# Kernel tuning notes

Hardware: AMD Instinct MI355X
Metric: run time of the kernel (lower is better)

## Reference

```python
import jax, jax.numpy as jnp
import numpy as np

N_NODES = 100000
N_EDGES = 2000000
IN_C = 30
OUT_C = 10
HID = 4 * OUT_C      # 40
D1 = 2 * OUT_C       # 20
D2 = OUT_C           # 10
N_CLASSES = 3
K_SAMPLE = 8


def setup_inputs() -> dict:
    key = jax.random.key(0)
    ks = jax.random.split(key, 24)
    inp = {
        'x': jax.random.normal(ks[0], (N_NODES, IN_C), dtype=jnp.float32),
        'edge_index': jax.random.randint(ks[1], (2, N_EDGES), 0, N_NODES, dtype=jnp.int64),
        'edge_attr': jax.random.uniform(ks[2], (N_EDGES,), dtype=jnp.float32),
        'label': 1,
        # gcn1
        'W1': jax.random.normal(ks[3], (IN_C, HID), dtype=jnp.float32) * (1.0 / np.sqrt(IN_C)),
        'b1': jnp.zeros((HID,), jnp.float32),
        'ln1_w': jnp.ones((HID,), jnp.float32),
        'ln1_b': jnp.zeros((HID,), jnp.float32),
        # gcn2
        'W2': jax.random.normal(ks[4], (HID, HID), dtype=jnp.float32) * (1.0 / np.sqrt(HID)),
        'b2': jnp.zeros((HID,), jnp.float32),
        'ln2_w': jnp.ones((HID,), jnp.float32),
        'ln2_b': jnp.zeros((HID,), jnp.float32),
        # fnn
        'Wf': jax.random.normal(ks[5], (HID, D1), dtype=jnp.float32) * (1.0 / np.sqrt(HID)),
        'bf': jnp.zeros((D1,), jnp.float32),
        # attention (tanh / sigmoid branches + concat)
        'Wt': jax.random.normal(ks[6], (D1, D2), dtype=jnp.float32) * (1.0 / np.sqrt(D1)),
        'bt': jnp.zeros((D2,), jnp.float32),
        'Ws': jax.random.normal(ks[7], (D1, D2), dtype=jnp.float32) * (1.0 / np.sqrt(D1)),
        'bs': jnp.zeros((D2,), jnp.float32),
        'Wc': jax.random.normal(ks[8], (D2, 1), dtype=jnp.float32) * (1.0 / np.sqrt(D2)),
        'bc': jnp.zeros((1,), jnp.float32),
        # bag classifier
        'Wcls': jax.random.normal(ks[9], (D1, N_CLASSES), dtype=jnp.float32) * (1.0 / np.sqrt(D1)),
        'bcls': jnp.zeros((N_CLASSES,), jnp.float32),
        # per-class cell-scale classifiers, stacked [n_classes, D1, 2]
        'Wcell': jax.random.normal(ks[10], (N_CLASSES, D1, 2), dtype=jnp.float32) * (1.0 / np.sqrt(D1)),
        'bcell': jnp.zeros((N_CLASSES, 2), jnp.float32),
    }
    return inp


def _layernorm(x, w, b, eps=1e-5):
    m = jnp.mean(x, axis=-1, keepdims=True)
    v = jnp.var(x, axis=-1, keepdims=True)
    return (x - m) * jax.lax.rsqrt(v + eps) * w + b


def _gcn(x, W, b, src, dst, ew, n):
    # PyG GCNConv: add self-loops (weight 1), symmetric norm, aggregate at dst
    h = x @ W                                              # [N, F]
    deg = jax.ops.segment_sum(ew, dst, num_segments=n) + 1.0
    dinv = jnp.where(deg > 0, jax.lax.rsqrt(deg), 0.0)     # [N]
    norm = dinv[src] * ew * dinv[dst]                      # [E]
    agg = jax.ops.segment_sum(h[src] * norm[:, None], dst, num_segments=n)
    agg = agg + h * (dinv * dinv)[:, None]                 # self-loop term
    return agg + b


def _forward(x, edge_attr, W1, b1, ln1_w, ln1_b, W2, b2, ln2_w, ln2_b,
             Wf, bf, Wt, bt, Ws, bs, Wc, bc, Wcls, bcls, Wcell, bcell,
             edge_index, label):
    src, dst = edge_index[0], edge_index[1]
    n = x.shape[0]
    x1 = jax.nn.selu(_layernorm(_gcn(x, W1, b1, src, dst, edge_attr, n), ln1_w, ln1_b))
    x2 = jax.nn.selu(_layernorm(_gcn(x1, W2, b2, src, dst, edge_attr, n), ln2_w, ln2_b))
    x3 = jax.nn.selu(x2 @ Wf + bf)                         # [N, D1] == x_out
    # gated tanh*sigmoid attention
    gate = jnp.tanh(x3 @ Wt + bt) * jax.nn.sigmoid(x3 @ Ws + bs)
    A = (gate @ Wc + bc).T                                 # [1, N]
    A = jax.nn.softmax(A, axis=1)
    # cell-scale eval for the true class (one-hot label selects exactly one)
    a_row = A[-1]                                          # [N]
    _, idx_p = jax.lax.top_k(a_row, K_SAMPLE)
    _, idx_n = jax.lax.top_k(-a_row, K_SAMPLE)
    all_cells = jnp.concatenate([x3[idx_p], x3[idx_n]], axis=0)   # [2K, D1]
    logits_c = all_cells @ Wcell[label] + bcell[label]            # [2K, 2]
    targets = jnp.concatenate([jnp.ones((K_SAMPLE,), jnp.int32),
                               jnp.zeros((K_SAMPLE,), jnp.int32)])
    # SmoothTop1SVM (tau=1, alpha=1): mean( logsumexp(s + Delta) - s_y )
    delta = 1.0 - jax.nn.one_hot(targets, 2, dtype=logits_c.dtype)
    s_y = jnp.take_along_axis(logits_c, targets[:, None], axis=1)[:, 0]
    cell_loss = jnp.mean(jax.nn.logsumexp(logits_c + delta, axis=1) - s_y)
    # bag-level prediction
    x_pooled = A @ x3                                      # [1, D1]
    logits = x_pooled @ Wcls + bcls                        # [1, n_classes]
    Y_prob = jax.nn.softmax(logits, axis=1)
    Y_hat = jnp.argmax(logits, axis=1)[:, None]
    return logits, Y_prob, Y_hat, A, x3, cell_loss


def reference(x, edge_index, edge_attr, label, W1, b1, ln1_w, ln1_b, W2, b2,
              ln2_w, ln2_b, Wf, bf, Wt, bt, Ws, bs, Wc, bc, Wcls, bcls,
              Wcell, bcell):
    return _forward(x, edge_attr, W1, b1, ln1_w, ln1_b, W2, b2, ln2_w, ln2_b,
                    Wf, bf, Wt, bt, Ws, bs, Wc, bc, Wcls, bcls, Wcell, bcell,
                    edge_index, label)
```

## Files before the change

kernel.cpp:

```cpp
#include <hip/hip_runtime.h>
#include <hip/hip_bf16.h>
#include <math.h>

typedef __hip_bfloat16 bf16;

__device__ __forceinline__ float tof(bf16 v){ return __bfloat162float(v); }
__device__ __forceinline__ bf16  tob(float v){ return __float2bfloat16(v); }

__device__ __forceinline__ float sane(float v){
  return (v == v && v > -1e30f && v < 1e30f) ? v : 0.f;
}
__device__ __forceinline__ float ldf(const void* p, size_t i, bool f32){
  float v = f32 ? ((const float*)p)[i] : tof(((const bf16*)p)[i]);
  return sane(v);
}
__device__ __forceinline__ void stf(void* p, size_t i, float v, bool f32){
  if (f32) ((float*)p)[i] = v; else ((bf16*)p)[i] = tob(v);
}
__device__ __forceinline__ bool is_f32(const unsigned* __restrict__ dt){
  return dt[0] == 0x3F800000u;
}
__device__ __forceinline__ int clampi(int v, int hi){
  return ((unsigned)v < (unsigned)hi) ? v : 0;
}
__device__ __forceinline__ float selu_f(float x){
  const float sc = 1.0507009873554805f, al = 1.6732632423543772f;
  return x > 0.f ? sc * x : sc * al * (expf(x) - 1.0f);
}
__device__ __forceinline__ void unpack8(uint4 u, float* f){
  f[0]=__uint_as_float(u.x<<16); f[1]=__uint_as_float(u.x&0xFFFF0000u);
  f[2]=__uint_as_float(u.y<<16); f[3]=__uint_as_float(u.y&0xFFFF0000u);
  f[4]=__uint_as_float(u.z<<16); f[5]=__uint_as_float(u.z&0xFFFF0000u);
  f[6]=__uint_as_float(u.w<<16); f[7]=__uint_as_float(u.w&0xFFFF0000u);
}
__device__ __forceinline__ void unpack4(uint2 u, float* f){
  f[0]=__uint_as_float(u.x<<16); f[1]=__uint_as_float(u.x&0xFFFF0000u);
  f[2]=__uint_as_float(u.y<<16); f[3]=__uint_as_float(u.y&0xFFFF0000u);
}
__device__ __forceinline__ unsigned pack2(float a, float b){
  unsigned short ua, ub;
  bf16 ta = tob(a), tb = tob(b);
  __builtin_memcpy(&ua, &ta, 2);
  __builtin_memcpy(&ub, &tb, 2);
  return (unsigned)ua | ((unsigned)ub << 16);
}

__global__ void k_zero(float* __restrict__ p, int n){
  int i = blockIdx.x * blockDim.x + threadIdx.x;
  int stride = gridDim.x * blockDim.x;
  for (; i < n; i += stride) p[i] = 0.f;
}

__device__ __forceinline__ bool idx_is64(const int* __restrict__ raw){
  return ((raw[1] | raw[3] | raw[5] | raw[7] | raw[9] | raw[11]) == 0);
}
__device__ __forceinline__ void edge_at(const int* __restrict__ raw, int E, int e,
                                        bool w64, int N, int& s, int& d){
  int sv, dv;
  if (w64){ sv = raw[2 * e]; dv = raw[2 * (E + e)]; }
  else    { sv = raw[e];     dv = raw[E + e]; }
  s = clampi(sv, N); d = clampi(dv, N);
}

__global__ void k_cnt_rank(const int* __restrict__ raw, int* __restrict__ cnt,
                           int* __restrict__ rank, int E, int N){
  int e = blockIdx.x * blockDim.x + threadIdx.x;
  if (e >= E) return;
  bool w64 = idx_is64(raw);
  int s, d; edge_at(raw, E, e, w64, N, s, d);
  rank[e] = atomicAdd(&cnt[d], 1);
}

__global__ void k_scan_block(const int* __restrict__ cnt, int* __restrict__ bsum, int N){
  __shared__ int s[256];
  int base = blockIdx.x * 1024;
  int acc = 0;
  for (int k = threadIdx.x; k < 1024; k += 256){
    int i = base + k;
    acc += (i < N) ? cnt[i] : 0;
  }
  s[threadIdx.x] = acc; __syncthreads();
  for (int w = 128; w > 0; w >>= 1){
    if (threadIdx.x < w) s[threadIdx.x] += s[threadIdx.x + w];
    __syncthreads();
  }
  if (threadIdx.x == 0) bsum[blockIdx.x] = s[0];
}

__global__ void k_scan_partials(int* __restrict__ bsum, int B, int* __restrict__ rowpN, int E){
  __shared__ int s[256];
  int run = 0;
  for (int t0 = 0; t0 < B; t0 += 256){
    int i = t0 + threadIdx.x;
    int v = (i < B) ? bsum[i] : 0;
    s[threadIdx.x] = v;
    __syncthreads();
    for (int o = 1; o < 256; o <<= 1){
      int add = (threadIdx.x >= o) ? s[threadIdx.x - o] : 0;
      __syncthreads();
      s[threadIdx.x] += add;
      __syncthreads();
    }
    int incl = s[threadIdx.x];
    int total = s[255];
    __syncthreads();
    if (i < B) bsum[i] = run + incl - v;
    run += total;
    __syncthreads();
  }
  if (threadIdx.x == 0) rowpN[0] = E;
}

__global__ void k_scan_final(const int* __restrict__ cnt, const int* __restrict__ bsum,
                             int* __restrict__ rowp, int N){
  __shared__ int s[256];
  int t = threadIdx.x;
  int base = bsum[blockIdx.x];
  int i0 = blockIdx.x * 1024 + t * 4;
  int v0=0,v1=0,v2=0,v3=0;
  if (i0+0 < N) v0 = cnt[i0+0];
  if (i0+1 < N) v1 = cnt[i0+1];
  if (i0+2 < N) v2 = cnt[i0+2];
  if (i0+3 < N) v3 = cnt[i0+3];
  int sum = v0+v1+v2+v3;
  s[t] = sum; __syncthreads();
  for (int o = 1; o < 256; o <<= 1){
    int add = (t >= o) ? s[t - o] : 0;
    __syncthreads();
    s[t] += add;
    __syncthreads();
  }
  int off = base + s[t] - sum;
  if (i0+0 < N){ rowp[i0+0]=off; off+=v0; }
  if (i0+1 < N){ rowp[i0+1]=off; off+=v1; }
  if (i0+2 < N){ rowp[i0+2]=off; off+=v2; }
  if (i0+3 < N){ rowp[i0+3]=off; off+=v3; }
}

__global__ void k_place(const int* __restrict__ raw, const void* __restrict__ ea,
                        const unsigned* __restrict__ dt, const int* __restrict__ rank,
                        const int* __restrict__ rowp, int2* __restrict__ ep, int E, int N){
  int e = blockIdx.x * blockDim.x + threadIdx.x;
  if (e >= E) return;
  bool f32 = is_f32(dt);
  bool w64 = idx_is64(raw);
  int s, d; edge_at(raw, E, e, w64, N, s, d);
  float w = ldf(ea, e, f32);
  int pos = rowp[d] + rank[e];
  if ((unsigned)pos < (unsigned)E)
    ep[pos] = make_int2(s, __float_as_int(w));
}

__global__ void k_dinv_csr(const int* __restrict__ rowp, const int2* __restrict__ ep,
                           float* __restrict__ dinv, int N, int E){
  int n = blockIdx.x * blockDim.x + threadIdx.x;
  if (n >= N) return;
  int beg = rowp[n], end = rowp[n + 1];
  if (beg < 0) beg = 0;
  if (end > E) end = E;
  float s = 0.f;
  for (int j = beg; j < end; j++) s += sane(__int_as_float(ep[j].y));
  float dv = s + 1.0f;
  dinv[n] = (dv > 0.f) ? rsqrtf(dv) : 0.f;
}

__global__ void k_premul(int2* __restrict__ ep, const float* __restrict__ dinv,
                         int E, int N){
  int i = blockIdx.x * blockDim.x + threadIdx.x;
  if (i >= E) return;
  int2 p = ep[i];
  int s = clampi(p.x, N);
  float w = dinv[s] * sane(__int_as_float(p.y));
  ep[i] = make_int2(s, __float_as_int(w));
}

__global__ void k_mm1(const void* __restrict__ X, const void* __restrict__ W,
                      const unsigned* __restrict__ dt,
                      bf16* __restrict__ H, int N, int Nx){
  bool f32 = is_f32(dt);
  __shared__ float w[30 * 40];
  __shared__ float xs[256 * 30];
  for (int i = threadIdx.x; i < 30 * 40; i += 256) w[i] = ldf(W, i, f32);
  int base = blockIdx.x * 256;
  int rows = Nx - base; if (rows > 256) rows = 256; if (rows < 0) rows = 0;
  int nelem = rows * 30;
  size_t gbase = (size_t)base * 30;
  for (int i = threadIdx.x; i < nelem; i += 256) xs[i] = ldf(X, gbase + i, f32);
  __syncthreads();
  int n = base + threadIdx.x;
  if (n >= N) return;
  float acc[40];
  #pragma unroll
  for (int j = 0; j < 40; j++) acc[j] = 0.f;
  if (threadIdx.x < rows){
    const float* xr = &xs[threadIdx.x * 30];
    for (int i = 0; i < 30; i++){
      float xi = xr[i];
      #pragma unroll
      for (int j = 0; j < 40; j++) acc[j] += xi * w[i * 40 + j];
    }
  } else {
    for (int i = 0; i < 30; i++){
      float xi = ldf(X, i, f32);
      #pragma unroll
      for (int j = 0; j < 40; j++) acc[j] += xi * w[i * 40 + j];
    }
  }
  uint4 ob[5];
  unsigned* ou = (unsigned*)ob;
  #pragma unroll
  for (int q = 0; q < 20; q++) ou[q] = pack2(acc[2*q], acc[2*q+1]);
  uint4* op = (uint4*)(H + (size_t)n * 40);
  #pragma unroll
  for (int q = 0; q < 5; q++) op[q] = ob[q];
}

__global__ void k_mm2(const bf16* __restrict__ X, const void* __restrict__ W,
                      const unsigned* __restrict__ dt,
                      bf16* __restrict__ H, int N){
  bool f32 = is_f32(dt);
  __shared__ float w[40 * 40];
  for (int i = threadIdx.x; i < 40 * 40; i += 256) w[i] = ldf(W, i, f32);
  __syncthreads();
  int n = blockIdx.x * blockDim.x + threadIdx.x;
  if (n >= N) return;
  float acc[40];
  #pragma unroll
  for (int j = 0; j < 40; j++) acc[j] = 0.f;
  const uint4* xp = (const uint4*)(X + (size_t)n * 40);
  #pragma unroll
  for (int q = 0; q < 5; q++){
    uint4 u = xp[q];
    float f[8]; unpack8(u, f);
    #pragma unroll
    for (int k = 0; k < 8; k++){
      float xi = f[k];
      int i = q * 8 + k;
      #pragma unroll
      for (int j = 0; j < 40; j++) acc[j] += xi * w[i * 40 + j];
    }
  }
  uint4 ob[5];
  unsigned* ou = (unsigned*)ob;
  #pragma unroll
  for (int q = 0; q < 20; q++) ou[q] = pack2(acc[2*q], acc[2*q+1]);
  uint4* op = (uint4*)(H + (size_t)n * 40);
  #pragma unroll
  for (int q = 0; q < 5; q++) op[q] = ob[q];
}

__global__ void k_gather(const int* __restrict__ rowp, const int2* __restrict__ ep,
                         const bf16* __restrict__ h, const float* __restrict__ dinv,
                         const void* __restrict__ b, const void* __restrict__ lw,
                         const void* __restrict__ lb, const unsigned* __restrict__ dt,
                         bf16* __restrict__ xout, int N, int E){
  int tid = blockIdx.x * blockDim.x + threadIdx.x;
  int n  = tid >> 3;
  int sl = tid & 7;
  if (n >= N) return;
  bool f32 = is_f32(dt);
  bool act = sl < 5;
  int fb = sl * 8;
  float dn = dinv[n];
  int beg = rowp[n], end = rowp[n + 1];
  if (beg < 0) beg = 0;
  if (end > E) end = E;
  float a[8];
  #pragma unroll
  for (int k = 0; k < 8; k++) a[k] = 0.f;
  int j = beg;
  for (; j + 3 < end; j += 4){
    int2 p0 = ep[j], p1 = ep[j+1], p2 = ep[j+2], p3 = ep[j+3];
    int s0 = clampi(p0.x, N), s1 = clampi(p1.x, N);
    int s2 = clampi(p2.x, N), s3 = clampi(p3.x, N);
    if (act){
      uint4 u0 = *(const uint4*)(h + (size_t)s0 * 40 + fb);
      uint4 u1 = *(const uint4*)(h + (size_t)s1 * 40 + fb);
      uint4 u2 = *(const uint4*)(h + (size_t)s2 * 40 + fb);
      uint4 u3 = *(const uint4*)(h + (size_t)s3 * 40 + fb);
      float w0 = __int_as_float(p0.y), w1 = __int_as_float(p1.y);
      float w2 = __int_as_float(p2.y), w3 = __int_as_float(p3.y);
      float f0[8], f1[8], f2[8], f3[8];
      unpack8(u0, f0); unpack8(u1, f1); unpack8(u2, f2); unpack8(u3, f3);
      #pragma unroll
      for (int k = 0; k < 8; k++)
        a[k] += f0[k]*w0 + f1[k]*w1 + f2[k]*w2 + f3[k]*w3;
    }
  }
  for (; j < end; j++){
    int2 p = ep[j];
    int s = clampi(p.x, N);
    if (act){
      uint4 u = *(const uint4*)(h + (size_t)s * 40 + fb);
      float w = __int_as_float(p.y);
      float f[8]; unpack8(u, f);
      #pragma unroll
      for (int k = 0; k < 8; k++) a[k] += f[k] * w;
    }
  }
  float v[8]; float psum = 0.f;
  if (act){
    uint4 us = *(const uint4*)(h + (size_t)n * 40 + fb);
    float fs[8]; unpack8(us, fs);
    float di2 = dn * dn;
    #pragma unroll
    for (int k = 0; k < 8; k++){
      v[k] = sane(a[k] * dn) + fs[k] * di2 + ldf(b, fb + k, f32);
      psum += v[k];
    }
  } else {
    #pragma unroll
    for (int k = 0; k < 8; k++) v[k] = 0.f;
  }
  float sum = psum;
  sum += __shfl_xor(sum, 1); sum += __shfl_xor(sum, 2); sum += __shfl_xor(sum, 4);
  float m = sum * (1.0f / 40.0f);
  float sq = 0.f;
  if (act){
    #pragma unroll
    for (int k = 0; k < 8; k++){ float d = v[k] - m; sq += d * d; }
  }
  sq += __shfl_xor(sq, 1); sq += __shfl_xor(sq, 2); sq += __shfl_xor(sq, 4);
  float inv = rsqrtf(sq * (1.0f / 40.0f) + 1e-5f);
  if (act){
    float y[8];
    #pragma unroll
    for (int k = 0; k < 8; k++)
      y[k] = sane(selu_f((v[k] - m) * inv * ldf(lw, fb + k, f32) + ldf(lb, fb + k, f32)));
    uint4 ob;
    unsigned* ou = (unsigned*)&ob;
    #pragma unroll
    for (int q = 0; q < 4; q++) ou[q] = pack2(y[2*q], y[2*q+1]);
    *(uint4*)(xout + (size_t)n * 40 + fb) = ob;
  }
}

__global__ void k_head(const bf16* __restrict__ x2,
                       const void* __restrict__ Wf, const void* __restrict__ bfv,
                       const void* __restrict__ Wt, const void* __restrict__ bt,
                       const void* __restrict__ Ws, const void* __restrict__ bs,
                       const void* __restrict__ Wc, const void* __restrict__ bc,
                       const unsigned* __restrict__ dt,
                       bf16* __restrict__ x3ws, float* __restrict__ alog, int N){
  bool f32 = is_f32(dt);
  __shared__ float wf[800], bff[20], wt[200], btt[10], wss[200], bss[10], wc[10], bcc[1];
  for (int i = threadIdx.x; i < 800; i += blockDim.x) wf[i] = ldf(Wf, i, f32);
  for (int i = threadIdx.x; i < 200; i += blockDim.x){
    wt[i] = ldf(Wt, i, f32); wss[i] = ldf(Ws, i, f32);
  }
  if (threadIdx.x < 20) bff[threadIdx.x] = ldf(bfv, threadIdx.x, f32);
  if (threadIdx.x < 10){ btt[threadIdx.x] = ldf(bt, threadIdx.x, f32);
                         bss[threadIdx.x] = ldf(bs, threadIdx.x, f32);
                         wc[threadIdx.x]  = ldf(Wc, threadIdx.x, f32); }
  if (threadIdx.x == 0) bcc[0] = ldf(bc, 0, f32);
  __syncthreads();
  int n = blockIdx.x * blockDim.x + threadIdx.x;
  if (n >= N) return;
  float r[40];
  const uint4* xp = (const uint4*)(x2 + (size_t)n * 40);
  #pragma unroll
  for (int q = 0; q < 5; q++){
    uint4 u = xp[q];
    unpack8(u, &r[q * 8]);
  }
  float x3r[20];
  #pragma unroll
  for (int j = 0; j < 20; j++){
    float acc = bff[j];
    for (int i = 0; i < 40; i++) acc += r[i] * wf[i * 20 + j];
    x3r[j] = sane(selu_f(acc));
  }
  uint2 ob[5];
  unsigned* ou = (unsigned*)ob;
  #pragma unroll
  for (int q = 0; q < 10; q++) ou[q] = pack2(x3r[2*q], x3r[2*q+1]);
  uint2* op = (uint2*)(x3ws + (size_t)n * 20);
  #pragma unroll
  for (int q = 0; q < 5; q++) op[q] = ob[q];
  float a = bcc[0];
  #pragma unroll
  for (int j = 0; j < 10; j++){
    float zt = btt[j], zs = bss[j];
    for (int i = 0; i < 20; i++){ zt += x3r[i] * wt[i * 10 + j]; zs += x3r[i] * wss[i * 10 + j]; }
    float g = tanhf(zt) * (1.0f / (1.0f + expf(-zs)));
    a += g * wc[j];
  }
  alog[n] = sane(a);
}

__global__ void k_copy_x3(const bf16* __restrict__ x3ws, const unsigned* __restrict__ dt,
                          void* __restrict__ out, size_t off, int total){
  bool f32 = is_f32(dt);
  int i = blockIdx.x * blockDim.x + threadIdx.x;
  int stride = gridDim.x * blockDim.x;
  for (; i < total; i += stride) stf(out, off + i, tof(x3ws[i]), f32);
}

__global__ void k_msum(const float* __restrict__ a, float2* __restrict__ part, int n){
  __shared__ float sm[256], sl[256];
  int t = threadIdx.x;
  float m = -1e30f, l = 0.f;
  for (int i = blockIdx.x * blockDim.x + t; i < n; i += gridDim.x * blockDim.x){
    float v = sane(a[i]);
    if (v > m){ l = l * expf(m - v) + 1.f; m = v; }
    else        l += expf(v - m);
  }
  sm[t] = m; sl[t] = l; __syncthreads();
  for (int w = 128; w > 0; w >>= 1){
    if (t < w){
      float m2 = sm[t+w], l2 = sl[t+w];
      float mm = fmaxf(sm[t], m2);
      sl[t] = sl[t] * expf(sm[t] - mm) + l2 * expf(m2 - mm);
      sm[t] = mm;
    }
    __syncthreads();
  }
  if (t == 0) part[blockIdx.x] = make_float2(sm[0], sl[0]);
}

__global__ void k_msum_fin(const float2* __restrict__ part, float* __restrict__ scal,
                           float* __restrict__ pooled){
  __shared__ float sm[256], sl[256];
  int t = threadIdx.x;
  float2 p = part[t];
  sm[t] = p.x; sl[t] = p.y; __syncthreads();
  for (int w = 128; w > 0; w >>= 1){
    if (t < w){
      float m2 = sm[t+w], l2 = sl[t+w];
      float mm = fmaxf(sm[t], m2);
      sl[t] = sl[t] * expf(sm[t] - mm) + l2 * expf(m2 - mm);
      sm[t] = mm;
    }
    __syncthreads();
  }
  if (t == 0){ scal[0] = sm[0]; scal[1] = sl[0]; }
  if (t < 20) pooled[t] = 0.f;
}

__global__ void k_writeA(const float* __restrict__ alog, const bf16* __restrict__ x3ws,
                         const float* __restrict__ scal,
                         const unsigned* __restrict__ dt,
                         void* __restrict__ out, size_t a_off,
                         float* __restrict__ pooled, int N){
  bool f32 = is_f32(dt);
  float gmax = scal[0];
  float sum  = scal[1];
  float inv  = (sum > 0.f) ? 1.0f / sum : 0.f;
  float acc[20];
  #pragma unroll
  for (int j = 0; j < 20; j++) acc[j] = 0.f;
  for (int i = blockIdx.x * blockDim.x + threadIdx.x; i < N; i += gridDim.x * blockDim.x){
    float a = expf(sane(alog[i]) - gmax) * inv;
    stf(out, a_off + i, a, f32);
    const uint2* xr = (const uint2*)(x3ws + (size_t)i * 20);
    #pragma unroll
    for (int q = 0; q < 5; q++){
      float f[4]; unpack4(xr[q], f);
      #pragma unroll
      for (int k = 0; k < 4; k++) acc[q * 4 + k] += a * f[k];
    }
  }
  __shared__ float s[20];
  if (threadIdx.x < 20) s[threadIdx.x] = 0.f;
  __syncthreads();
  #pragma unroll
  for (int j = 0; j < 20; j++) atomicAdd(&s[j], acc[j]);
  __syncthreads();
  if (threadIdx.x < 20) atomicAdd(&pooled[threadIdx.x], s[threadIdx.x]);
}

__global__ void k_topk1(const float* __restrict__ a, int N,
                        float* __restrict__ cvp, int* __restrict__ cip,
                        float* __restrict__ cvn, int* __restrict__ cin){
  const int T = 256, K = 8;
  __shared__ float sv[T * K];
  __shared__ int   si[T * K];
  __shared__ float rv[T];
  __shared__ int   ri[T];
  __shared__ int   rs[T];
  int t = threadIdx.x;
  float tv[K]; int ti[K]; float bv[K]; int bi[K];
  #pragma unroll
  for (int k = 0; k < K; k++){ tv[k] = -1e38f; ti[k] = 0x7ffffff;
                               bv[k] =  1e38f; bi[k] = 0x7ffffff; }
  for (int i = blockIdx.x * T + t; i < N; i += gridDim.x * T){
    float v = sane(a[i]);
    if (v > tv[K-1]){
      int p = K - 1;
      while (p > 0 && v > tv[p-1]){ tv[p] = tv[p-1]; ti[p] = ti[p-1]; p--; }
      tv[p] = v; ti[p] = i;
    }
    if (v < bv[K-1]){
      int p = K - 1;
      while (p > 0 && v < bv[p-1]){ bv[p] = bv[p-1]; bi[p] = bi[p-1]; p--; }
      bv[p] = v; bi[p] = i;
    }
  }
  for (int k = 0; k < K; k++){ sv[t*K+k] = tv[k]; si[t*K+k] = ti[k]; }
  __syncthreads();
  for (int round = 0; round < K; round++){
    float bvv = -1e38f; int bii = 0x7ffffff; int bslot = 0;
    for (int k = 0; k < K; k++){
      float v = sv[t*K+k]; int ii = si[t*K+k];
      if (v > bvv || (v == bvv && ii < bii)){ bvv = v; bii = ii; bslot = t*K+k; }
    }
    rv[t] = bvv; ri[t] = bii; rs[t] = bslot;
    __syncthreads();
    for (int w = T/2; w > 0; w >>= 1){
      if (t < w){
        float v2 = rv[t+w]; int i2 = ri[t+w];
        if (v2 > rv[t] || (v2 == rv[t] && i2 < ri[t])){ rv[t]=v2; ri[t]=i2; rs[t]=rs[t+w]; }
      }
      __syncthreads();
    }
    if (t == 0){ cvp[blockIdx.x*K + round] = rv[0]; cip[blockIdx.x*K + round] = ri[0];
                 sv[rs[0]] = -1e38f; }
    __syncthreads();
  }
  for (int k = 0; k < K; k++){ sv[t*K+k] = bv[k]; si[t*K+k] = bi[k]; }
  __syncthreads();
  for (int round = 0; round < K; round++){
    float bvv = 1e38f; int bii = 0x7ffffff; int bslot = 0;
    for (int k = 0; k < K; k++){
      float v = sv[t*K+k]; int ii = si[t*K+k];
      if (v < bvv || (v == bvv && ii < bii)){ bvv = v; bii = ii; bslot = t*K+k; }
    }
    rv[t] = bvv; ri[t] = bii; rs[t] = bslot;
    __syncthreads();
    for (int w = T/2; w > 0; w >>= 1){
      if (t < w){
        float v2 = rv[t+w]; int i2 = ri[t+w];
        if (v2 < rv[t] || (v2 == rv[t] && i2 < ri[t])){ rv[t]=v2; ri[t]=i2; rs[t]=rs[t+w]; }
      }
      __syncthreads();
    }
    if (t == 0){ cvn[blockIdx.x*K + round] = rv[0]; cin[blockIdx.x*K + round] = ri[0];
                 sv[rs[0]] = 1e38f; }
    __syncthreads();
  }
}

__global__ void k_topk2(const float* __restrict__ cvp, const int* __restrict__ cip,
                        const float* __restrict__ cvn, const int* __restrict__ cin,
                        int* __restrict__ idxp, int* __restrict__ idxn, int M){
  const int T = 256, CAP = 1024, PER = CAP / T;
  __shared__ float sv[CAP];
  __shared__ int   si[CAP];
  __shared__ float rv[T];
  __shared__ int   ri[T];
  __shared__ int   rs[T];
  int t = threadIdx.x;
  for (int i = t; i < CAP; i += T){
    sv[i] = (i < M) ? cvp[i] : -1e38f;
    si[i] = (i < M) ? cip[i] : 0x7ffffff;
  }
  __syncthreads();
  for (int round = 0; round < 8; round++){
    float bvv = -1e38f; int bii = 0x7ffffff; int bslot = t * PER;
    for (int k = 0; k < PER; k++){
      float v = sv[t*PER+k]; int ii = si[t*PER+k];
      if (v > bvv || (v == bvv && ii < bii)){ bvv = v; bii = ii; bslot = t*PER+k; }
    }
    rv[t] = bvv; ri[t] = bii; rs[t] = bslot;
    __syncthreads();
    for (int w = T/2; w > 0; w >>= 1){
      if (t < w){
        float v2 = rv[t+w]; int i2 = ri[t+w];
        if (v2 > rv[t] || (v2 == rv[t] && i2 < ri[t])){ rv[t]=v2; ri[t]=i2; rs[t]=rs[t+w]; }
      }
      __syncthreads();
    }
    if (t == 0){ idxp[round] = ri[0]; sv[rs[0]] = -1e38f; }
    __syncthreads();
  }
  for (int i = t; i < CAP; i += T){
    sv[i] = (i < M) ? cvn[i] : 1e38f;
    si[i] = (i < M) ? cin[i] : 0x7ffffff;
  }
  __syncthreads();
  for (int round = 0; round < 8; round++){
    float bvv = 1e38f; int bii = 0x7ffffff; int bslot = t * PER;
    for (int k = 0; k < PER; k++){
      float v = sv[t*PER+k]; int ii = si[t*PER+k];
      if (v < bvv || (v == bvv && ii < bii)){ bvv = v; bii = ii; bslot = t*PER+k; }
    }
    rv[t] = bvv; ri[t] = bii; rs[t] = bslot;
    __syncthreads();
    for (int w = T/2; w > 0; w >>= 1){
      if (t < w){
        float v2 = rv[t+w]; int i2 = ri[t+w];
        if (v2 < rv[t] || (v2 == rv[t] && i2 < ri[t])){ rv[t]=v2; ri[t]=i2; rs[t]=rs[t+w]; }
      }
      __syncthreads();
    }
    if (t == 0){ idxn[round] = ri[0]; sv[rs[0]] = 1e38f; }
    __syncthreads();
  }
}

__global__ void k_final(const float* __restrict__ pooled,
                        const void* __restrict__ Wcls, const void* __restrict__ bcls,
                        const void* __restrict__ Wcell, const void* __restrict__ bcell,
                        const int* __restrict__ label_p, const bf16* __restrict__ x3ws,
                        const int* __restrict__ idxp, const int* __restrict__ idxn,
                        const unsigned* __restrict__ dt,
                        void* __restrict__ out, int N){
  if (threadIdx.x != 0 || blockIdx.x != 0) return;
  bool f32 = is_f32(dt);
  float lg[3];
  for (int c = 0; c < 3; c++){
    float acc = ldf(bcls, c, f32);
    for (int j = 0; j < 20; j++) acc += sane(pooled[j]) * ldf(Wcls, j * 3 + c, f32);
    lg[c] = sane(acc);
  }
  float m = fmaxf(lg[0], fmaxf(lg[1], lg[2]));
  float e0 = expf(lg[0]-m), e1 = expf(lg[1]-m), e2 = expf(lg[2]-m);
  float es = e0 + e1 + e2;
  int yhat = 0;
  if (lg[1] > lg[yhat]) yhat = 1;
  if (lg[2] > lg[yhat]) yhat = 2;
  stf(out, 0, lg[0], f32); stf(out, 1, lg[1], f32); stf(out, 2, lg[2], f32);
  stf(out, 3, e0/es, f32); stf(out, 4, e1/es, f32); stf(out, 5, e2/es, f32);
  stf(out, 6, (float)yhat, f32);
  int lw0 = label_p[0];
  int label;
  if ((unsigned)lw0 < 3u) label = lw0;
  else if (lw0 == 0x3F800000 || lw0 == 0x3F803F80) label = 1;
  else if (lw0 == 0x40000000 || lw0 == 0x40004000) label = 2;
  else label = 0;
  float w0[20], w1[20];
  for (int j = 0; j < 20; j++){
    w0[j] = ldf(Wcell, (size_t)label * 40 + j*2 + 0, f32);
    w1[j] = ldf(Wcell, (size_t)label * 40 + j*2 + 1, f32);
  }
  float b0 = ldf(bcell, (size_t)label * 2 + 0, f32);
  float b1 = ldf(bcell, (size_t)label * 2 + 1, f32);
  float loss = 0.f;
  for (int i = 0; i < 16; i++){
    int node = clampi((i < 8) ? idxp[i] : idxn[i-8], N);
    const bf16* xr = x3ws + (size_t)node * 20;
    float l0 = b0, l1 = b1;
    for (int j = 0; j < 20; j++){ float xv = tof(xr[j]); l0 += xv * w0[j]; l1 += xv * w1[j]; }
    int tgt = (i < 8) ? 1 : 0;
    float a0 = l0 + ((tgt == 0) ? 0.f : 1.f);
    float a1 = l1 + ((tgt == 1) ? 0.f : 1.f);
    float mm = fmaxf(a0, a1);
    float lse = mm + logf(expf(a0-mm) + expf(a1-mm));
    float sy = tgt ? l1 : l0;
    loss += lse - sy;
  }
  stf(out, (size_t)7 + N + (size_t)20 * N, sane(loss * (1.0f / 16.0f)), f32);
}

extern "C" void kernel_launch(void* const* d_in, const int* in_sizes, int n_in,
                              void* d_out, int out_size, void* d_ws, size_t ws_size,
                              hipStream_t stream) {
  const int N = (out_size - 8) / 21;
  if (N <= 0) return;
  const int Nx = (in_sizes[0] / 30 < N) ? (in_sizes[0] / 30) : N;
  int E = in_sizes[1] / 2;
  if (in_sizes[2] < E) E = in_sizes[2];
  if (E < 6) return;

  const void* x    = d_in[0];
  const int*  eraw = (const int*)d_in[1];
  const void* ea   = d_in[2];
  const int*  lbl  = (const int*)d_in[3];
  const void* W1   = d_in[4];
  const void* b1   = d_in[5];
  const unsigned* dt = (const unsigned*)d_in[6];
  const void* ln1w = d_in[6];
  const void* ln1b = d_in[7];
  const void* W2   = d_in[8];
  const void* b2   = d_in[9];
  const void* ln2w = d_in[10];
  const void* ln2b = d_in[11];
  const void* Wf   = d_in[12];
  const void* bfv  = d_in[13];
  const void* Wt   = d_in[14];
  const void* bt   = d_in[15];
  const void* Ws   = d_in[16];
  const void* bs   = d_in[17];
  const void* Wc   = d_in[18];
  const void* bc   = d_in[19];
  const void* Wcls = d_in[20];
  const void* bcls = d_in[21];
  const void* Wcell= d_in[22];
  const void* bcell= d_in[23];

  auto align16 = [](size_t v){ return (v + 15) & ~(size_t)15; };
  size_t hA_bytes = (size_t)N * 40 * 2;
  size_t rank_bytes = (size_t)E * 4;
  size_t regA = hA_bytes > rank_bytes ? hA_bytes : rank_bytes;
  size_t off = 0;
  char* ws = (char*)d_ws;
  bf16* hA    = (bf16*)(ws + off);
  int*  rank  = (int*)(ws + off);  off = align16(off + regA);
  bf16* xB    = (bf16*)(ws + off); off = align16(off + (size_t)N * 40 * 2);
  int2* epack = (int2*)(ws + off); off = align16(off + (size_t)E * 8);
  int*  rowp  = (int*)(ws + off);  off = align16(off + (size_t)(N + 1) * 4);
  int*  cnt   = (int*)(ws + off);  off = align16(off + (size_t)N * 4);
  int*  bsum  = (int*)(ws + off);  off = align16(off + 4096 * 4);
  float* dinv = (float*)(ws + off); off = align16(off + (size_t)N * 4);
  float* alog = (float*)(ws + off); off = align16(off + (size_t)N * 4);
  float2* part2 = (float2*)(ws + off); off = align16(off + 256 * 8);
  float* scal = (float*)(ws + off); off = align16(off + 2 * 4);
  float* pooled = (float*)(ws + off); off = align16(off + 20 * 4);
  int*   idxp = (int*)(ws + off); off = align16(off + 8 * 4);
  int*   idxn = (int*)(ws + off); off = align16(off + 8 * 4);
  float* cvp  = (float*)(ws + off); off = align16(off + 1024 * 4);
  int*   cip  = (int*)(ws + off);   off = align16(off + 1024 * 4);
  float* cvn  = (float*)(ws + off); off = align16(off + 1024 * 4);
  int*   cin  = (int*)(ws + off);   off = align16(off + 1024 * 4);
  if (off > ws_size) return;
  bf16* x3ws = hA;

  const int TB = 256;
  const int gN = (N + TB - 1) / TB;
  const int gE = (E + TB - 1) / TB;
  const int gG = (int)(((size_t)N * 8 + TB - 1) / TB);
  const int SB = (N + 1023) / 1024;
  const int TP = 128;

  k_zero<<<gN, TB, 0, stream>>>((float*)cnt, N);
  k_cnt_rank<<<gE, TB, 0, stream>>>(eraw, cnt, rank, E, N);
  k_scan_block<<<SB, TB, 0, stream>>>(cnt, bsum, N);
  k_scan_partials<<<1, TB, 0, stream>>>(bsum, SB, rowp + N, E);
  k_scan_final<<<SB, TB, 0, stream>>>(cnt, bsum, rowp, N);
  k_place<<<gE, TB, 0, stream>>>(eraw, ea, dt, rank, rowp, epack, E, N);
  k_dinv_csr<<<gN, TB, 0, stream>>>(rowp, epack, dinv, N, E);
  k_premul<<<gE, TB, 0, stream>>>(epack, dinv, E, N);

  k_mm1<<<gN, TB, 0, stream>>>(x, W1, dt, hA, N, Nx);
  k_gather<<<gG, TB, 0, stream>>>(rowp, epack, hA, dinv, b1, ln1w, ln1b, dt, xB, N, E);

  k_mm2<<<gN, TB, 0, stream>>>(xB, W2, dt, hA, N);
  k_gather<<<gG, TB, 0, stream>>>(rowp, epack, hA, dinv, b2, ln2w, ln2b, dt, xB, N, E);

  k_head<<<gN, TB, 0, stream>>>(xB, Wf, bfv, Wt, bt, Ws, bs, Wc, bc, dt,
                                x3ws, alog, N);
  k_copy_x3<<<2048, TB, 0, stream>>>(x3ws, dt, d_out, (size_t)7 + N, 20 * N);

  k_msum<<<256, TB, 0, stream>>>(alog, part2, N);
  k_msum_fin<<<1, TB, 0, stream>>>(part2, scal, pooled);
  k_writeA<<<256, TB, 0, stream>>>(alog, x3ws, scal, dt, d_out, (size_t)7, pooled, N);

  k_topk1<<<TP, TB, 0, stream>>>(alog, N, cvp, cip, cvn, cin);
  k_topk2<<<1, TB, 0, stream>>>(cvp, cip, cvn, cin, idxp, idxn, TP * 8);
  k_final<<<1, 64, 0, stream>>>(pooled, Wcls, bcls, Wcell, bcell, lbl,
                                x3ws, idxp, idxn, dt, d_out, N);
}
```

Baseline: 602.2 us.

## Fold dinv premultiply into gather and fuse softmax-stats with top-k selection

Measured after the change: 592.0 us. Within noise of the previous version (-1.7%).

```diff
diff --git a/kernel.cpp b/kernel.cpp
--- a/kernel.cpp
+++ b/kernel.cpp
@@ -162,16 +162,6 @@
   for (int j = beg; j < end; j++) s += sane(__int_as_float(ep[j].y));
   float dv = s + 1.0f;
   dinv[n] = (dv > 0.f) ? rsqrtf(dv) : 0.f;
-}
-
-__global__ void k_premul(int2* __restrict__ ep, const float* __restrict__ dinv,
-                         int E, int N){
-  int i = blockIdx.x * blockDim.x + threadIdx.x;
-  if (i >= E) return;
-  int2 p = ep[i];
-  int s = clampi(p.x, N);
-  float w = dinv[s] * sane(__int_as_float(p.y));
-  ep[i] = make_int2(s, __float_as_int(w));
 }
 
 __global__ void k_mm1(const void* __restrict__ X, const void* __restrict__ W,
@@ -273,13 +263,15 @@
     int2 p0 = ep[j], p1 = ep[j+1], p2 = ep[j+2], p3 = ep[j+3];
     int s0 = clampi(p0.x, N), s1 = clampi(p1.x, N);
     int s2 = clampi(p2.x, N), s3 = clampi(p3.x, N);
+    float w0 = dinv[s0] * __int_as_float(p0.y);
+    float w1 = dinv[s1] * __int_as_float(p1.y);
+    float w2 = dinv[s2] * __int_as_float(p2.y);
+    float w3 = dinv[s3] * __int_as_float(p3.y);
     if (act){
       uint4 u0 = *(const uint4*)(h + (size_t)s0 * 40 + fb);
       uint4 u1 = *(const uint4*)(h + (size_t)s1 * 40 + fb);
       uint4 u2 = *(const uint4*)(h + (size_t)s2 * 40 + fb);
       uint4 u3 = *(const uint4*)(h + (size_t)s3 * 40 + fb);
-      float w0 = __int_as_float(p0.y), w1 = __int_as_float(p1.y);
-      float w2 = __int_as_float(p2.y), w3 = __int_as_float(p3.y);
       float f0[8], f1[8], f2[8], f3[8];
       unpack8(u0, f0); unpack8(u1, f1); unpack8(u2, f2); unpack8(u3, f3);
       #pragma unroll
@@ -290,9 +282,9 @@
   for (; j < end; j++){
     int2 p = ep[j];
     int s = clampi(p.x, N);
+    float w = dinv[s] * __int_as_float(p.y);
     if (act){
       uint4 u = *(const uint4*)(h + (size_t)s * 40 + fb);
-      float w = __int_as_float(p.y);
       float f[8]; unpack8(u, f);
       #pragma unroll
       for (int k = 0; k < 8; k++) a[k] += f[k] * w;
@@ -396,45 +388,167 @@
   for (; i < total; i += stride) stf(out, off + i, tof(x3ws[i]), f32);
 }
 
-__global__ void k_msum(const float* __restrict__ a, float2* __restrict__ part, int n){
-  __shared__ float sm[256], sl[256];
+__global__ void k_msum_topk1(const float* __restrict__ a, int N,
+                             float2* __restrict__ part,
+                             float* __restrict__ cvp, int* __restrict__ cip,
+                             float* __restrict__ cvn, int* __restrict__ cin){
+  const int T = 256, K = 8;
+  __shared__ float sv[T * K];
+  __shared__ int   si[T * K];
+  __shared__ float rv[T];
+  __shared__ int   ri[T];
+  __shared__ int   rs[T];
+  __shared__ float sm[T], slh[T];
   int t = threadIdx.x;
   float m = -1e30f, l = 0.f;
-  for (int i = blockIdx.x * blockDim.x + t; i < n; i += gridDim.x * blockDim.x){
+  float tv[K]; int ti[K]; float bv[K]; int bi[K];
+  #pragma unroll
+  for (int k = 0; k < K; k++){ tv[k] = -1e38f; ti[k] = 0x7ffffff;
+                               bv[k] =  1e38f; bi[k] = 0x7ffffff; }
+  for (int i = blockIdx.x * T + t; i < N; i += gridDim.x * T){
     float v = sane(a[i]);
     if (v > m){ l = l * expf(m - v) + 1.f; m = v; }
     else        l += expf(v - m);
-  }
-  sm[t] = m; sl[t] = l; __syncthreads();
+    if (v > tv[K-1]){
+      int p = K - 1;
+      while (p > 0 && v > tv[p-1]){ tv[p] = tv[p-1]; ti[p] = ti[p-1]; p--; }
+      tv[p] = v; ti[p] = i;
+    }
+    if (v < bv[K-1]){
+      int p = K - 1;
+      while (p > 0 && v < bv[p-1]){ bv[p] = bv[p-1]; bi[p] = bi[p-1]; p--; }
+      bv[p] = v; bi[p] = i;
+    }
+  }
+  sm[t] = m; slh[t] = l; __syncthreads();
   for (int w = 128; w > 0; w >>= 1){
     if (t < w){
-      float m2 = sm[t+w], l2 = sl[t+w];
+      float m2 = sm[t+w], l2 = slh[t+w];
       float mm = fmaxf(sm[t], m2);
-      sl[t] = sl[t] * expf(sm[t] - mm) + l2 * expf(m2 - mm);
+      slh[t] = slh[t] * expf(sm[t] - mm) + l2 * expf(m2 - mm);
       sm[t] = mm;
     }
     __syncthreads();
   }
-  if (t == 0) part[blockIdx.x] = make_float2(sm[0], sl[0]);
-}
-
-__global__ void k_msum_fin(const float2* __restrict__ part, float* __restrict__ scal,
-                           float* __restrict__ pooled){
-  __shared__ float sm[256], sl[256];
+  if (t == 0) part[blockIdx.x] = make_float2(sm[0], slh[0]);
+  __syncthreads();
+  for (int k = 0; k < K; k++){ sv[t*K+k] = tv[k]; si[t*K+k] = ti[k]; }
+  __syncthreads();
+  for (int round = 0; round < K; round++){
+    float bvv = -1e38f; int bii = 0x7ffffff; int bslot = 0;
+    for (int k = 0; k < K; k++){
+      float v = sv[t*K+k]; int ii = si[t*K+k];
+      if (v > bvv || (v == bvv && ii < bii)){ bvv = v; bii = ii; bslot = t*K+k; }
+    }
+    rv[t] = bvv; ri[t] = bii; rs[t] = bslot;
+    __syncthreads();
+    for (int w = T/2; w > 0; w >>= 1){
+      if (t < w){
+        float v2 = rv[t+w]; int i2 = ri[t+w];
+        if (v2 > rv[t] || (v2 == rv[t] && i2 < ri[t])){ rv[t]=v2; ri[t]=i2; rs[t]=rs[t+w]; }
+      }
+      __syncthreads();
+    }
+    if (t == 0){ cvp[blockIdx.x*K + round] = rv[0]; cip[blockIdx.x*K + round] = ri[0];
+                 sv[rs[0]] = -1e38f; }
+    __syncthreads();
+  }
+  for (int k = 0; k < K; k++){ sv[t*K+k] = bv[k]; si[t*K+k] = bi[k]; }
+  __syncthreads();
+  for (int round = 0; round < K; round++){
+    float bvv = 1e38f; int bii = 0x7ffffff; int bslot = 0;
+    for (int k = 0; k < K; k++){
+      float v = sv[t*K+k]; int ii = si[t*K+k];
+      if (v < bvv || (v == bvv && ii < bii)){ bvv = v; bii = ii; bslot = t*K+k; }
+    }
+    rv[t] = bvv; ri[t] = bii; rs[t] = bslot;
+    __syncthreads();
+    for (int w = T/2; w > 0; w >>= 1){
+      if (t < w){
+        float v2 = rv[t+w]; int i2 = ri[t+w];
+        if (v2 < rv[t] || (v2 == rv[t] && i2 < ri[t])){ rv[t]=v2; ri[t]=i2; rs[t]=rs[t+w]; }
+      }
+      __syncthreads();
+    }
+    if (t == 0){ cvn[blockIdx.x*K + round] = rv[0]; cin[blockIdx.x*K + round] = ri[0];
+                 sv[rs[0]] = 1e38f; }
+    __syncthreads();
+  }
+}
+
+__global__ void k_fin(const float2* __restrict__ part, int P,
+                      const float* __restrict__ cvp, const int* __restrict__ cip,
+                      const float* __restrict__ cvn, const int* __restrict__ cin,
+                      float* __restrict__ scal, float* __restrict__ pooled,
+                      int* __restrict__ idxp, int* __restrict__ idxn, int M){
+  const int T = 256, CAP = 1024, PER = CAP / T;
+  __shared__ float sv[CAP];
+  __shared__ int   si[CAP];
+  __shared__ float rv[T];
+  __shared__ int   ri[T];
+  __shared__ int   rs[T];
   int t = threadIdx.x;
-  float2 p = part[t];
-  sm[t] = p.x; sl[t] = p.y; __syncthreads();
+  float m = -1e30f, l = 0.f;
+  if (t < P){ float2 p = part[t]; m = p.x; l = p.y; }
+  rv[t] = m; sv[t] = l; __syncthreads();
   for (int w = 128; w > 0; w >>= 1){
     if (t < w){
-      float m2 = sm[t+w], l2 = sl[t+w];
-      float mm = fmaxf(sm[t], m2);
-      sl[t] = sl[t] * expf(sm[t] - mm) + l2 * expf(m2 - mm);
-      sm[t] = mm;
-    }
-    __syncthreads();
-  }
-  if (t == 0){ scal[0] = sm[0]; scal[1] = sl[0]; }
+      float m2 = rv[t+w], l2 = sv[t+w];
+      float mm = fmaxf(rv[t], m2);
+      sv[t] = sv[t] * expf(rv[t] - mm) + l2 * expf(m2 - mm);
+      rv[t] = mm;
+    }
+    __syncthreads();
+  }
+  if (t == 0){ scal[0] = rv[0]; scal[1] = sv[0]; }
   if (t < 20) pooled[t] = 0.f;
+  __syncthreads();
+  for (int i = t; i < CAP; i += T){
+    sv[i] = (i < M) ? cvp[i] : -1e38f;
+    si[i] = (i < M) ? cip[i] : 0x7ffffff;
+  }
+  __syncthreads();
+  for (int round = 0; round < 8; round++){
+    float bvv = -1e38f; int bii = 0x7ffffff; int bslot = t * PER;
+    for (int k = 0; k < PER; k++){
+      float v = sv[t*PER+k]; int ii = si[t*PER+k];
+      if (v > bvv || (v == bvv && ii < bii)){ bvv = v; bii = ii; bslot = t*PER+k; }
+    }
+    rv[t] = bvv; ri[t] = bii; rs[t] = bslot;
+    __syncthreads();
+    for (int w = T/2; w > 0; w >>= 1){
+      if (t < w){
+        float v2 = rv[t+w]; int i2 = ri[t+w];
+        if (v2 > rv[t] || (v2 == rv[t] && i2 < ri[t])){ rv[t]=v2; ri[t]=i2; rs[t]=rs[t+w]; }
+      }
+      __syncthreads();
+    }
+    if (t == 0){ idxp[round] = ri[0]; sv[rs[0]] = -1e38f; }
+    __syncthreads();
+  }
+  for (int i = t; i < CAP; i += T){
+    sv[i] = (i < M) ? cvn[i] : 1e38f;
+    si[i] = (i < M) ? cin[i] : 0x7ffffff;
+  }
+  __syncthreads();
+  for (int round = 0; round < 8; round++){
+    float bvv = 1e38f; int bii = 0x7ffffff; int bslot = t * PER;
+    for (int k = 0; k < PER; k++){
+      float v = sv[t*PER+k]; int ii = si[t*PER+k];
+      if (v < bvv || (v == bvv && ii < bii)){ bvv = v; bii = ii; bslot = t*PER+k; }
+    }
+    rv[t] = bvv; ri[t] = bii; rs[t] = bslot;
+    __syncthreads();
+    for (int w = T/2; w > 0; w >>= 1){
+      if (t < w){
+        float v2 = rv[t+w]; int i2 = ri[t+w];
+        if (v2 < rv[t] || (v2 == rv[t] && i2 < ri[t])){ rv[t]=v2; ri[t]=i2; rs[t]=rs[t+w]; }
+      }
+      __syncthreads();
+    }
+    if (t == 0){ idxn[round] = ri[0]; sv[rs[0]] = 1e38f; }
+    __syncthreads();
+  }
 }
 
 __global__ void k_writeA(const float* __restrict__ alog, const bf16* __restrict__ x3ws,
@@ -467,135 +581,6 @@
   for (int j = 0; j < 20; j++) atomicAdd(&s[j], acc[j]);
   __syncthreads();
   if (threadIdx.x < 20) atomicAdd(&pooled[threadIdx.x], s[threadIdx.x]);
-}
-
-__global__ void k_topk1(const float* __restrict__ a, int N,
-                        float* __restrict__ cvp, int* __restrict__ cip,
-                        float* __restrict__ cvn, int* __restrict__ cin){
-  const int T = 256, K = 8;
-  __shared__ float sv[T * K];
-  __shared__ int   si[T * K];
-  __shared__ float rv[T];
-  __shared__ int   ri[T];
-  __shared__ int   rs[T];
-  int t = threadIdx.x;
-  float tv[K]; int ti[K]; float bv[K]; int bi[K];
-  #pragma unroll
-  for (int k = 0; k < K; k++){ tv[k] = -1e38f; ti[k] = 0x7ffffff;
-                               bv[k] =  1e38f; bi[k] = 0x7ffffff; }
-  for (int i = blockIdx.x * T + t; i < N; i += gridDim.x * T){
-    float v = sane(a[i]);
-    if (v > tv[K-1]){
-      int p = K - 1;
-      while (p > 0 && v > tv[p-1]){ tv[p] = tv[p-1]; ti[p] = ti[p-1]; p--; }
-      tv[p] = v; ti[p] = i;
-    }
-    if (v < bv[K-1]){
-      int p = K - 1;
-      while (p > 0 && v < bv[p-1]){ bv[p] = bv[p-1]; bi[p] = bi[p-1]; p--; }
-      bv[p] = v; bi[p] = i;
-    }
-  }
-  for (int k = 0; k < K; k++){ sv[t*K+k] = tv[k]; si[t*K+k] = ti[k]; }
-  __syncthreads();
-  for (int round = 0; round < K; round++){
-    float bvv = -1e38f; int bii = 0x7ffffff; int bslot = 0;
-    for (int k = 0; k < K; k++){
-      float v = sv[t*K+k]; int ii = si[t*K+k];
-      if (v > bvv || (v == bvv && ii < bii)){ bvv = v; bii = ii; bslot = t*K+k; }
-    }
-    rv[t] = bvv; ri[t] = bii; rs[t] = bslot;
-    __syncthreads();
-    for (int w = T/2; w > 0; w >>= 1){
-      if (t < w){
-        float v2 = rv[t+w]; int i2 = ri[t+w];
-        if (v2 > rv[t] || (v2 == rv[t] && i2 < ri[t])){ rv[t]=v2; ri[t]=i2; rs[t]=rs[t+w]; }
-      }
-      __syncthreads();
-    }
-    if (t == 0){ cvp[blockIdx.x*K + round] = rv[0]; cip[blockIdx.x*K + round] = ri[0];
-                 sv[rs[0]] = -1e38f; }
-    __syncthreads();
-  }
-  for (int k = 0; k < K; k++){ sv[t*K+k] = bv[k]; si[t*K+k] = bi[k]; }
-  __syncthreads();
-  for (int round = 0; round < K; round++){
-    float bvv = 1e38f; int bii = 0x7ffffff; int bslot = 0;
-    for (int k = 0; k < K; k++){
-      float v = sv[t*K+k]; int ii = si[t*K+k];
-      if (v < bvv || (v == bvv && ii < bii)){ bvv = v; bii = ii; bslot = t*K+k; }
-    }
-    rv[t] = bvv; ri[t] = bii; rs[t] = bslot;
-    __syncthreads();
-    for (int w = T/2; w > 0; w >>= 1){
-      if (t < w){
-        float v2 = rv[t+w]; int i2 = ri[t+w];
-        if (v2 < rv[t] || (v2 == rv[t] && i2 < ri[t])){ rv[t]=v2; ri[t]=i2; rs[t]=rs[t+w]; }
-      }
-      __syncthreads();
-    }
-    if (t == 0){ cvn[blockIdx.x*K + round] = rv[0]; cin[blockIdx.x*K + round] = ri[0];
-                 sv[rs[0]] = 1e38f; }
-    __syncthreads();
-  }
-}
-
-__global__ void k_topk2(const float* __restrict__ cvp, const int* __restrict__ cip,
-                        const float* __restrict__ cvn, const int* __restrict__ cin,
-                        int* __restrict__ idxp, int* __restrict__ idxn, int M){
-  const int T = 256, CAP = 1024, PER = CAP / T;
-  __shared__ float sv[CAP];
-  __shared__ int   si[CAP];
-  __shared__ float rv[T];
-  __shared__ int   ri[T];
-  __shared__ int   rs[T];
-  int t = threadIdx.x;
-  for (int i = t; i < CAP; i += T){
-    sv[i] = (i < M) ? cvp[i] : -1e38f;
-    si[i] = (i < M) ? cip[i] : 0x7ffffff;
-  }
-  __syncthreads();
-  for (int round = 0; round < 8; round++){
-    float bvv = -1e38f; int bii = 0x7ffffff; int bslot = t * PER;
-    for (int k = 0; k < PER; k++){
-      float v = sv[t*PER+k]; int ii = si[t*PER+k];
-      if (v > bvv || (v == bvv && ii < bii)){ bvv = v; bii = ii; bslot = t*PER+k; }
-    }
-    rv[t] = bvv; ri[t] = bii; rs[t] = bslot;
-    __syncthreads();
-    for (int w = T/2; w > 0; w >>= 1){
-      if (t < w){
-        float v2 = rv[t+w]; int i2 = ri[t+w];
-        if (v2 > rv[t] || (v2 == rv[t] && i2 < ri[t])){ rv[t]=v2; ri[t]=i2; rs[t]=rs[t+w]; }
-      }
-      __syncthreads();
-    }
-    if (t == 0){ idxp[round] = ri[0]; sv[rs[0]] = -1e38f; }
-    __syncthreads();
-  }
-  for (int i = t; i < CAP; i += T){
-    sv[i] = (i < M) ? cvn[i] : 1e38f;
-    si[i] = (i < M) ? cin[i] : 0x7ffffff;
-  }
-  __syncthreads();
-  for (int round = 0; round < 8; round++){
-    float bvv = 1e38f; int bii = 0x7ffffff; int bslot = t * PER;
-    for (int k = 0; k < PER; k++){
-      float v = sv[t*PER+k]; int ii = si[t*PER+k];
-      if (v < bvv || (v == bvv && ii < bii)){ bvv = v; bii = ii; bslot = t*PER+k; }
-    }
-    rv[t] = bvv; ri[t] = bii; rs[t] = bslot;
-    __syncthreads();
-    for (int w = T/2; w > 0; w >>= 1){
-      if (t < w){
-        float v2 = rv[t+w]; int i2 = ri[t+w];
-        if (v2 < rv[t] || (v2 == rv[t] && i2 < ri[t])){ rv[t]=v2; ri[t]=i2; rs[t]=rs[t+w]; }
-      }
-      __syncthreads();
-    }
-    if (t == 0){ idxn[round] = ri[0]; sv[rs[0]] = 1e38f; }
-    __syncthreads();
-  }
 }
 
 __global__ void k_final(const float* __restrict__ pooled,
@@ -729,7 +714,6 @@
   k_scan_final<<<SB, TB, 0, stream>>>(cnt, bsum, rowp, N);
   k_place<<<gE, TB, 0, stream>>>(eraw, ea, dt, rank, rowp, epack, E, N);
   k_dinv_csr<<<gN, TB, 0, stream>>>(rowp, epack, dinv, N, E);
-  k_premul<<<gE, TB, 0, stream>>>(epack, dinv, E, N);
 
   k_mm1<<<gN, TB, 0, stream>>>(x, W1, dt, hA, N, Nx);
   k_gather<<<gG, TB, 0, stream>>>(rowp, epack, hA, dinv, b1, ln1w, ln1b, dt, xB, N, E);
@@ -741,12 +725,10 @@
                                 x3ws, alog, N);
   k_copy_x3<<<2048, TB, 0, stream>>>(x3ws, dt, d_out, (size_t)7 + N, 20 * N);
 
-  k_msum<<<256, TB, 0, stream>>>(alog, part2, N);
-  k_msum_fin<<<1, TB, 0, stream>>>(part2, scal, pooled);
+  k_msum_topk1<<<TP, TB, 0, stream>>>(alog, N, part2, cvp, cip, cvn, cin);
+  k_fin<<<1, TB, 0, stream>>>(part2, TP, cvp, cip, cvn, cin,
+                              scal, pooled, idxp, idxn, TP * 8);
   k_writeA<<<256, TB, 0, stream>>>(alog, x3ws, scal, dt, d_out, (size_t)7, pooled, N);
-
-  k_topk1<<<TP, TB, 0, stream>>>(alog, N, cvp, cip, cvn, cin);
-  k_topk2<<<1, TB, 0, stream>>>(cvp, cip, cvn, cin, idxp, idxn, TP * 8);
   k_final<<<1, 64, 0, stream>>>(pooled, Wcls, bcls, Wcell, bcell, lbl,
                                 x3ws, idxp, idxn, dt, d_out, N);
 }
```
